# Kernel tuning notes

Hardware: AMD Instinct MI355X
Metric: run time of the kernel (lower is better)

Reference implementation:

```python
import jax, jax.numpy as jnp
import numpy as np

S_STATES, C_TYPES, G_GENES = 16, 64, 20000


def setup_inputs() -> dict:
    key = jax.random.key(0)
    k1, k2, k3, k4 = jax.random.split(key, 4)
    Z_mu = jax.random.normal(k1, (C_TYPES, G_GENES), dtype=jnp.float32)
    # positive log-normal sigmas, moderate scale for numerical stability
    Z_sigma = jax.random.uniform(k2, (C_TYPES, G_GENES), dtype=jnp.float32) * 0.5 + 0.1
    # build a valid correlation matrix (PSD with unit diagonal) so var >= 0
    L = jax.random.normal(k3, (C_TYPES, C_TYPES), dtype=jnp.float32)
    cov = L @ L.T + C_TYPES * jnp.eye(C_TYPES, dtype=jnp.float32)
    d = jnp.sqrt(jnp.diag(cov))
    corr = cov / (d[:, None] * d[None, :])
    # cell_prob rows on the simplex (Dirichlet-like), per state
    cell_prob = jax.nn.softmax(jax.random.normal(k4, (S_STATES, C_TYPES), dtype=jnp.float32), axis=1)
    return {"Z_mu": Z_mu, "Z_sigma": Z_sigma, "corr": corr, "cell_prob": cell_prob}


def reference(Z_mu, Z_sigma, corr, cell_prob):
    """Vectorized LogNorm.calculate_mu_sigma.

    Z_mu, Z_sigma: (C, G); corr: (C, C); cell_prob: (S, C).
    Returns mu, sigma of shape (S, G) -- moment-matched log-normal sum params
    for every (state, gene) pair, matching the nested-loop torch original.
    """
    # EV[s,c,g] = exp(mu + sigma^2/2) * w  (first moment of each component, weighted)
    ev_base = jnp.exp(Z_mu + 0.5 * Z_sigma ** 2)            # (C, G)
    EV = cell_prob[:, :, None] * ev_base[None, :, :]         # (S, C, G)
    Ssum = EV.sum(axis=1)                                    # (S, G)
    # A[s,c,g] = EV * sigma; var = sum_{c,d} A_c corr_{cd} A_d / Ssum^2
    A = EV * Z_sigma[None, :, :]                             # (S, C, G)
    var = jnp.einsum('scg,cd,sdg->sg', A, corr, A) / (Ssum ** 2)  # (S, G)
    mu_s = jnp.log(Ssum) - 0.5 * var
    sigma_s = jnp.sqrt(var)
    return (mu_s, sigma_s)
```

## Files before the change

### kernel.cpp

```cpp
#include <hip/hip_runtime.h>


#define S_STATES 16
#define C_TYPES  64
#define G_GENES  20000
#define OUT_HALF (S_STATES * G_GENES)
#define NPAIR    96
#define PER_WAVE 24

typedef _Float16 f16x2 __attribute__((ext_vector_type(2)));
typedef _Float16 f16x8 __attribute__((ext_vector_type(8)));
typedef float    f32x4 __attribute__((ext_vector_type(4)));

union Frag8 { f16x2 p[4]; f16x8 v; uint4 u; _Float16 h[8]; };

__global__ __launch_bounds__(64)
void build_A(const float* __restrict__ corr, const float* __restrict__ w,
             unsigned short* __restrict__ cwA)
{
    const int p    = blockIdx.x;
    const int lane = threadIdx.x;
    const int gl   = lane & 15;
    const int q    = lane >> 4;
    Frag8 v;
    if (p < NPAIR) {
        const int dh = (p >= 64);
        const int c  = dh ? p - 32 : p;
        const int d0 = dh * 32 + q * 8;
        const float wc = w[gl * C_TYPES + c];
        const float4 c0 = *(const float4*)(corr + c * C_TYPES + d0);
        const float4 c1 = *(const float4*)(corr + c * C_TYPES + d0 + 4);
        const float4 w0 = *(const float4*)(w + gl * C_TYPES + d0);
        const float4 w1 = *(const float4*)(w + gl * C_TYPES + d0 + 4);
        const float cv[8] = {c0.x,c0.y,c0.z,c0.w,c1.x,c1.y,c1.z,c1.w};
        const float wv[8] = {w0.x,w0.y,w0.z,w0.w,w1.x,w1.y,w1.z,w1.w};
#pragma unroll
        for (int j = 0; j < 8; ++j) {
            const int d = d0 + j;
            const float sc = (d < c) ? 2.0f : (d == c ? 1.0f : 0.0f);
            v.h[j] = (_Float16)(sc * cv[j] * wc * wv[j]);
        }
    } else {
        const int k0 = (p - NPAIR) * 32 + q * 8;
        const float4 w0 = *(const float4*)(w + gl * C_TYPES + k0);
        const float4 w1 = *(const float4*)(w + gl * C_TYPES + k0 + 4);
        const float wv[8] = {w0.x,w0.y,w0.z,w0.w,w1.x,w1.y,w1.z,w1.w};
#pragma unroll
        for (int j = 0; j < 8; ++j) v.h[j] = (_Float16)wv[j];
    }
    *(uint4*)(cwA + (p << 9) + lane * 8) = v.u;
}

__global__ __launch_bounds__(256, 4)
void lognorm_main(const float* __restrict__ Z_mu,
                  const float* __restrict__ Z_sigma,
                  const unsigned short* __restrict__ cwA,
                  float* __restrict__ out)
{
    __shared__ f16x2 x2pT[32][35];
    __shared__ f16x2 x1pT[32][35];
    __shared__ f16x2 x2tp[C_TYPES][21];
    __shared__ float accs[4][S_STATES][33];
    __shared__ float ssum_s[S_STATES][33];

    const int gt    = blockIdx.x;
    const int tid   = threadIdx.x;
    const int w     = tid >> 6;
    const int lane  = tid & 63;
    const int gl    = lane & 15;
    const int q     = lane >> 4;
    const int gbase = gt * 32;

    {
        const int dp = tid >> 3;
        const int gq = tid & 7;
        const int ga = gq * 2;
        const float* zm0 = Z_mu    + (2*dp) * G_GENES + gbase + ga;
        const float* zs0 = Z_sigma + (2*dp) * G_GENES + gbase + ga;
        const float2 m00 = *(const float2*)zm0;
        const float2 m01 = *(const float2*)(zm0 + 16);
        const float2 m10 = *(const float2*)(zm0 + G_GENES);
        const float2 m11 = *(const float2*)(zm0 + G_GENES + 16);
        const float2 s00 = *(const float2*)zs0;
        const float2 s01 = *(const float2*)(zs0 + 16);
        const float2 s10 = *(const float2*)(zs0 + G_GENES);
        const float2 s11 = *(const float2*)(zs0 + G_GENES + 16);
        float x1v[2][2][2], x2v[2][2][2];
#define XDO(r,h,j,M,S) { const float s_=(S); const float e_=__expf(fmaf(0.5f*s_,s_,(M)))*0.25f; \
                         x1v[r][h][j]=e_; x2v[r][h][j]=e_*s_; }
        XDO(0,0,0, m00.x, s00.x) XDO(0,0,1, m00.y, s00.y)
        XDO(0,1,0, m01.x, s01.x) XDO(0,1,1, m01.y, s01.y)
        XDO(1,0,0, m10.x, s10.x) XDO(1,0,1, m10.y, s10.y)
        XDO(1,1,0, m11.x, s11.x) XDO(1,1,1, m11.y, s11.y)
#undef XDO
#pragma unroll
        for (int h = 0; h < 2; ++h)
#pragma unroll
            for (int j = 0; j < 2; ++j) {
                const int g = ga + j + 16 * h;
                f16x2 a, b;
                a.x = (_Float16)x2v[0][h][j]; a.y = (_Float16)x2v[1][h][j];
                b.x = (_Float16)x1v[0][h][j]; b.y = (_Float16)x1v[1][h][j];
                x2pT[g][dp] = a;
                x1pT[g][dp] = b;
            }
#pragma unroll
        for (int r = 0; r < 2; ++r)
#pragma unroll
            for (int j = 0; j < 2; ++j) {
                f16x2 a;
                a.x = (_Float16)x2v[r][0][j];
                a.y = (_Float16)x2v[r][1][j];
                x2tp[2*dp + r][ga + j] = a;
            }
    }
    __syncthreads();

    f16x2 xh[2][4][2];
#pragma unroll
    for (int dh = 0; dh < 2; ++dh)
#pragma unroll
        for (int t = 0; t < 2; ++t)
#pragma unroll
            for (int jp = 0; jp < 4; ++jp)
                xh[dh][jp][t] = x2pT[gl + 16*t][dh*16 + q*4 + jp];

    f16x2 xct[PER_WAVE];
#pragma unroll
    for (int i = 0; i < PER_WAVE; ++i) {
        const int c = i*4 + w - ((i >= 16) ? 32 : 0);
        xct[i] = x2tp[c][gl];
    }

    const unsigned short* Abase = cwA + (w << 9) + lane * 8;
    f32x4 acc0a = {0.f,0.f,0.f,0.f}, acc0b = {0.f,0.f,0.f,0.f};
    f32x4 acc1a = {0.f,0.f,0.f,0.f}, acc1b = {0.f,0.f,0.f,0.f};
#pragma unroll
    for (int i = 0; i < PER_WAVE; ++i) {
        Frag8 af; af.u = *(const uint4*)(Abase + (i << 11));
        const int dh = (i >= 16) ? 1 : 0;
        Frag8 b0, b1;
#pragma unroll
        for (int jp = 0; jp < 4; ++jp) {
            f16x2 s0; s0.x = xct[i].x; s0.y = xct[i].x;
            f16x2 s1; s1.x = xct[i].y; s1.y = xct[i].y;
            b0.p[jp] = s0 * xh[dh][jp][0];
            b1.p[jp] = s1 * xh[dh][jp][1];
        }
        if (i & 1) {
            acc0b = __builtin_amdgcn_mfma_f32_16x16x32_f16(af.v, b0.v, acc0b, 0, 0, 0);
            acc1b = __builtin_amdgcn_mfma_f32_16x16x32_f16(af.v, b1.v, acc1b, 0, 0, 0);
        } else {
            acc0a = __builtin_amdgcn_mfma_f32_16x16x32_f16(af.v, b0.v, acc0a, 0, 0, 0);
            acc1a = __builtin_amdgcn_mfma_f32_16x16x32_f16(af.v, b1.v, acc1a, 0, 0, 0);
        }
    }
    const f32x4 acc0 = acc0a + acc0b;
    const f32x4 acc1 = acc1a + acc1b;
#pragma unroll
    for (int r = 0; r < 4; ++r) {
        accs[w][q*4 + r][gl]      = acc0[r];
        accs[w][q*4 + r][gl + 16] = acc1[r];
    }

    if (w < 2) {
        Frag8 wf0, wf1;
        wf0.u = *(const uint4*)(cwA + ((NPAIR + 0) << 9) + lane * 8);
        wf1.u = *(const uint4*)(cwA + ((NPAIR + 1) << 9) + lane * 8);
        Frag8 x1f[2];
#pragma unroll
        for (int kk = 0; kk < 2; ++kk)
#pragma unroll
            for (int jp = 0; jp < 4; ++jp)
                x1f[kk].p[jp] = x1pT[gl + 16*w][kk*16 + q*4 + jp];
        f32x4 sa = {0.f,0.f,0.f,0.f};
        sa = __builtin_amdgcn_mfma_f32_16x16x32_f16(wf0.v, x1f[0].v, sa, 0, 0, 0);
        sa = __builtin_amdgcn_mfma_f32_16x16x32_f16(wf1.v, x1f[1].v, sa, 0, 0, 0);
#pragma unroll
        for (int r = 0; r < 4; ++r) ssum_s[q*4 + r][gl + 16*w] = sa[r];
    }
    __syncthreads();

    const int s  = tid >> 4;
    const int gx = tid & 15;
#pragma unroll
    for (int t = 0; t < 2; ++t) {
        const int gg = gx + 16 * t;
        const float vn = (accs[0][s][gg] + accs[1][s][gg])
                       + (accs[2][s][gg] + accs[3][s][gg]);
        const float ss   = ssum_s[s][gg];
        const float rvar = fmaxf(vn, 0.f) / (ss * ss);
        out[s * G_GENES + gbase + gg] =
            __logf(ss) + 1.3862943611f - 0.5f * rvar;
        out[OUT_HALF + s * G_GENES + gbase + gg] = sqrtf(rvar);
    }
}

extern "C" void kernel_launch(void* const* d_in, const int* in_sizes, int n_in,
                              void* d_out, int out_size, void* d_ws, size_t ws_size,
                              hipStream_t stream) {
    const float* Z_mu      = (const float*)d_in[0];
    const float* Z_sigma   = (const float*)d_in[1];
    const float* corr      = (const float*)d_in[2];
    const float* cell_prob = (const float*)d_in[3];
    float* out = (float*)d_out;
    unsigned short* cwA = (unsigned short*)d_ws;

    build_A<<<dim3(NPAIR + 2), dim3(64), 0, stream>>>(corr, cell_prob, cwA);

    const int gtiles = G_GENES / 32;
    lognorm_main<<<dim3(gtiles), dim3(256), 0, stream>>>(
        Z_mu, Z_sigma, cwA, out);
}
```

Before: 15.52 us.

## Split MFMA pair work across eight waves per block instead of four

Doubles the block to 512 threads so each wave handles 12 instead of 24 correlation-pair MFMA steps. The prologue and epilogue are reworked to match: each thread loads scalar inputs for one gene column, and each thread reduces eight partial accumulators for one output. The goal is to shorten the per-block serial MFMA chain and raise latency hiding, at the cost of more LDS for partial sums, a wider final reduction, and scalar rather than float2 global loads.

```diff
diff --git a/kernel.cpp b/kernel.cpp
--- a/kernel.cpp
+++ b/kernel.cpp
@@ -6,7 +6,7 @@
 #define G_GENES  20000
 #define OUT_HALF (S_STATES * G_GENES)
 #define NPAIR    96
-#define PER_WAVE 24
+#define PER_WAVE 12
 
 typedef _Float16 f16x2 __attribute__((ext_vector_type(2)));
 typedef _Float16 f16x8 __attribute__((ext_vector_type(8)));
@@ -51,7 +51,7 @@
     *(uint4*)(cwA + (p << 9) + lane * 8) = v.u;
 }
 
-__global__ __launch_bounds__(256, 4)
+__global__ __launch_bounds__(512, 6)
 void lognorm_main(const float* __restrict__ Z_mu,
                   const float* __restrict__ Z_sigma,
                   const unsigned short* __restrict__ cwA,
@@ -60,7 +60,7 @@
     __shared__ f16x2 x2pT[32][35];
     __shared__ f16x2 x1pT[32][35];
     __shared__ f16x2 x2tp[C_TYPES][21];
-    __shared__ float accs[4][S_STATES][33];
+    __shared__ float accs[8][S_STATES][33];
     __shared__ float ssum_s[S_STATES][33];
 
     const int gt    = blockIdx.x;
@@ -72,47 +72,27 @@
     const int gbase = gt * 32;
 
     {
-        const int dp = tid >> 3;
-        const int gq = tid & 7;
-        const int ga = gq * 2;
-        const float* zm0 = Z_mu    + (2*dp) * G_GENES + gbase + ga;
-        const float* zs0 = Z_sigma + (2*dp) * G_GENES + gbase + ga;
-        const float2 m00 = *(const float2*)zm0;
-        const float2 m01 = *(const float2*)(zm0 + 16);
-        const float2 m10 = *(const float2*)(zm0 + G_GENES);
-        const float2 m11 = *(const float2*)(zm0 + G_GENES + 16);
-        const float2 s00 = *(const float2*)zs0;
-        const float2 s01 = *(const float2*)(zs0 + 16);
-        const float2 s10 = *(const float2*)(zs0 + G_GENES);
-        const float2 s11 = *(const float2*)(zs0 + G_GENES + 16);
-        float x1v[2][2][2], x2v[2][2][2];
-#define XDO(r,h,j,M,S) { const float s_=(S); const float e_=__expf(fmaf(0.5f*s_,s_,(M)))*0.25f; \
-                         x1v[r][h][j]=e_; x2v[r][h][j]=e_*s_; }
-        XDO(0,0,0, m00.x, s00.x) XDO(0,0,1, m00.y, s00.y)
-        XDO(0,1,0, m01.x, s01.x) XDO(0,1,1, m01.y, s01.y)
-        XDO(1,0,0, m10.x, s10.x) XDO(1,0,1, m10.y, s10.y)
-        XDO(1,1,0, m11.x, s11.x) XDO(1,1,1, m11.y, s11.y)
-#undef XDO
-#pragma unroll
-        for (int h = 0; h < 2; ++h)
-#pragma unroll
-            for (int j = 0; j < 2; ++j) {
-                const int g = ga + j + 16 * h;
-                f16x2 a, b;
-                a.x = (_Float16)x2v[0][h][j]; a.y = (_Float16)x2v[1][h][j];
-                b.x = (_Float16)x1v[0][h][j]; b.y = (_Float16)x1v[1][h][j];
-                x2pT[g][dp] = a;
-                x1pT[g][dp] = b;
-            }
-#pragma unroll
-        for (int r = 0; r < 2; ++r)
-#pragma unroll
-            for (int j = 0; j < 2; ++j) {
-                f16x2 a;
-                a.x = (_Float16)x2v[r][0][j];
-                a.y = (_Float16)x2v[r][1][j];
-                x2tp[2*dp + r][ga + j] = a;
-            }
+        const int dp = tid >> 4;
+        const int gq = tid & 15;
+        const float* zm = Z_mu    + (2*dp) * G_GENES + gbase + gq;
+        const float* zs = Z_sigma + (2*dp) * G_GENES + gbase + gq;
+        const float m00 = zm[0], m01 = zm[16];
+        const float m10 = zm[G_GENES], m11 = zm[G_GENES + 16];
+        const float s00 = zs[0], s01 = zs[16];
+        const float s10 = zs[G_GENES], s11 = zs[G_GENES + 16];
+        const float e00 = __expf(fmaf(0.5f*s00, s00, m00)) * 0.25f;
+        const float e01 = __expf(fmaf(0.5f*s01, s01, m01)) * 0.25f;
+        const float e10 = __expf(fmaf(0.5f*s10, s10, m10)) * 0.25f;
+        const float e11 = __expf(fmaf(0.5f*s11, s11, m11)) * 0.25f;
+        const float x200 = e00*s00, x201 = e01*s01;
+        const float x210 = e10*s10, x211 = e11*s11;
+        f16x2 a;
+        a.x = (_Float16)x200; a.y = (_Float16)x210; x2pT[gq][dp]      = a;
+        a.x = (_Float16)x201; a.y = (_Float16)x211; x2pT[gq + 16][dp] = a;
+        a.x = (_Float16)e00;  a.y = (_Float16)e10;  x1pT[gq][dp]      = a;
+        a.x = (_Float16)e01;  a.y = (_Float16)e11;  x1pT[gq + 16][dp] = a;
+        a.x = (_Float16)x200; a.y = (_Float16)x201; x2tp[2*dp][gq]    = a;
+        a.x = (_Float16)x210; a.y = (_Float16)x211; x2tp[2*dp+1][gq]  = a;
     }
     __syncthreads();
 
@@ -128,7 +108,7 @@
     f16x2 xct[PER_WAVE];
 #pragma unroll
     for (int i = 0; i < PER_WAVE; ++i) {
-        const int c = i*4 + w - ((i >= 16) ? 32 : 0);
+        const int c = i*8 + w - ((i >= 8) ? 32 : 0);
         xct[i] = x2tp[c][gl];
     }
 
@@ -137,8 +117,8 @@
     f32x4 acc1a = {0.f,0.f,0.f,0.f}, acc1b = {0.f,0.f,0.f,0.f};
 #pragma unroll
     for (int i = 0; i < PER_WAVE; ++i) {
-        Frag8 af; af.u = *(const uint4*)(Abase + (i << 11));
-        const int dh = (i >= 16) ? 1 : 0;
+        Frag8 af; af.u = *(const uint4*)(Abase + (i << 12));
+        const int dh = (i >= 8) ? 1 : 0;
         Frag8 b0, b1;
 #pragma unroll
         for (int jp = 0; jp < 4; ++jp) {
@@ -181,19 +161,16 @@
     }
     __syncthreads();
 
-    const int s  = tid >> 4;
-    const int gx = tid & 15;
+    const int s  = tid >> 5;
+    const int gx = tid & 31;
+    float vn = 0.f;
 #pragma unroll
-    for (int t = 0; t < 2; ++t) {
-        const int gg = gx + 16 * t;
-        const float vn = (accs[0][s][gg] + accs[1][s][gg])
-                       + (accs[2][s][gg] + accs[3][s][gg]);
-        const float ss   = ssum_s[s][gg];
-        const float rvar = fmaxf(vn, 0.f) / (ss * ss);
-        out[s * G_GENES + gbase + gg] =
-            __logf(ss) + 1.3862943611f - 0.5f * rvar;
-        out[OUT_HALF + s * G_GENES + gbase + gg] = sqrtf(rvar);
-    }
+    for (int k = 0; k < 8; ++k) vn += accs[k][s][gx];
+    const float ss   = ssum_s[s][gx];
+    const float rvar = fmaxf(vn, 0.f) / (ss * ss);
+    out[s * G_GENES + gbase + gx] =
+        __logf(ss) + 1.3862943611f - 0.5f * rvar;
+    out[OUT_HALF + s * G_GENES + gbase + gx] = sqrtf(rvar);
 }
 
 extern "C" void kernel_launch(void* const* d_in, const int* in_sizes, int n_in,
@@ -209,6 +186,6 @@
     build_A<<<dim3(NPAIR + 2), dim3(64), 0, stream>>>(corr, cell_prob, cwA);
 
     const int gtiles = G_GENES / 32;
-    lognorm_main<<<dim3(gtiles), dim3(256), 0, stream>>>(
+    lognorm_main<<<dim3(gtiles), dim3(512), 0, stream>>>(
         Z_mu, Z_sigma, cwA, out);
 }
```

Result: no change. 15.60 us (+0.5%).
